# Optimization experiments

Hardware: AMD Instinct MI355X
Metric: run time of the kernel (lower is better)

The kernel has to match this reference:

```python
import jax, jax.numpy as jnp
import numpy as np

N = 100000      # nodes
E = 800000      # edges (avg degree 8)
D_IN = 64
H1 = H2 = H3 = 64
HEADS = 2
D_EDGE = 5
NEG_SLOPE = 0.2  # GATConv leaky_relu slope


def _lin(key, fi, fo):
    kw, kb = jax.random.split(key)
    w = jax.random.normal(kw, (fi, fo), jnp.float32) / np.sqrt(fi)
    b = jax.random.normal(kb, (fo,), jnp.float32) * 0.01
    return w, b


def setup_inputs() -> dict:
    key = jax.random.key(0)
    ks = jax.random.split(key, 16)
    x = jax.random.normal(ks[0], (N, D_IN), jnp.float32)
    edge_index = jax.random.randint(ks[1], (2, E), 0, N, dtype=jnp.int32)
    edge_attr = jax.random.normal(ks[2], (E, D_EDGE), jnp.float32)

    inp = {"x": x, "edge_index": edge_index, "edge_attr": edge_attr}
    dims = [(D_IN, H1), (H1, H2), (H2, H3)]
    for i, (fi, fo) in enumerate(dims, start=1):
        k = jax.random.fold_in(ks[3], i)
        ka, kb, kc = jax.random.split(k, 3)
        inp[f"w_node{i}"], inp[f"b_node{i}"] = _lin(ka, fi, fo)
        inp[f"w_edge{i}"], inp[f"b_edge{i}"] = _lin(kb, D_EDGE, fo)
        inp[f"w_comb{i}"], inp[f"b_comb{i}"] = _lin(kc, 2 * fo, fo)
    # GATConv: shared lin for src/dst, att vectors, bias (concat=False -> size H3)
    kg, ks_, kd, kbias = jax.random.split(ks[4], 4)
    inp["w_gat"] = jax.random.normal(kg, (H3, HEADS * H3), jnp.float32) / np.sqrt(H3)
    inp["att_src"] = jax.random.normal(ks_, (HEADS, H3), jnp.float32) * 0.1
    inp["att_dst"] = jax.random.normal(kd, (HEADS, H3), jnp.float32) * 0.1
    inp["b_gat"] = jax.random.normal(kbias, (H3,), jnp.float32) * 0.01
    return inp


def _edge_conv(h, src, dst, ea, wn, bn, we, be, wc, bc, n):
    # lin_node / lin_edge applied densely, then gather -> concat -> lin -> scatter-add
    hn = h @ wn + bn                       # [N, C]
    ef = ea @ we + be                      # [E, C]
    msg = jnp.concatenate([hn[src], ef], axis=1) @ wc + bc  # [E, C]
    return jax.ops.segment_sum(msg, dst, num_segments=n)


def _gat(h, src, dst, w_gat, att_src, att_dst, b_gat, n):
    g = (h @ w_gat).reshape(n, HEADS, -1)          # [N, H, C]
    a_src = jnp.einsum("nhc,hc->nh", g, att_src)    # [N, H]
    a_dst = jnp.einsum("nhc,hc->nh", g, att_dst)
    alpha = jax.nn.leaky_relu(a_src[src] + a_dst[dst], NEG_SLOPE)  # [E, H]
    # segment softmax over incoming edges of each dst node
    m = jax.ops.segment_max(alpha, dst, num_segments=n)
    alpha = jnp.exp(alpha - m[dst])
    denom = jax.ops.segment_sum(alpha, dst, num_segments=n)
    alpha = alpha / (denom[dst] + 1e-16)
    out = jax.ops.segment_sum(g[src] * alpha[:, :, None], dst, num_segments=n)  # [N,H,C]
    return out.mean(axis=1) + b_gat  # concat=False -> mean over heads, plus bias


def reference(x, edge_index, edge_attr,
              w_node1, b_node1, w_edge1, b_edge1, w_comb1, b_comb1,
              w_node2, b_node2, w_edge2, b_edge2, w_comb2, b_comb2,
              w_node3, b_node3, w_edge3, b_edge3, w_comb3, b_comb3,
              w_gat, att_src, att_dst, b_gat):
    n = x.shape[0]
    src, dst = edge_index[0], edge_index[1]
    h = x
    h = jax.nn.relu(_edge_conv(h, src, dst, edge_attr, w_node1, b_node1, w_edge1, b_edge1, w_comb1, b_comb1, n))
    h = jax.nn.relu(_edge_conv(h, src, dst, edge_attr, w_node2, b_node2, w_edge2, b_edge2, w_comb2, b_comb2, n))
    h = jax.nn.relu(_edge_conv(h, src, dst, edge_attr, w_node3, b_node3, w_edge3, b_edge3, w_comb3, b_comb3, n))
    h = _gat(h, src, dst, w_gat, att_src, att_dst, b_gat, n)
    return h.reshape(-1)  # torch.flatten
```

## Files before the change

kernel.cpp:

```cpp
#include <hip/hip_runtime.h>
#include <hip/hip_fp16.h>
#include <math.h>


#define TPB 256

typedef unsigned int u32;

__device__ inline float2 f16unpack2(u32 u) {
    __half2 h = *reinterpret_cast<__half2*>(&u);
    return __half22float2(h);
}
__device__ inline float4 f16unpack4(uint2 q) {
    float2 a = f16unpack2(q.x), b = f16unpack2(q.y);
    return make_float4(a.x, a.y, b.x, b.y);
}
__device__ inline u32 f16pack2(float lo, float hi) {
    __half2 h = __floats2half2_rn(lo, hi);
    return *reinterpret_cast<u32*>(&h);
}
__device__ inline void fma_f16x8(float* acc, uint4 v, float w) {
    float2 t;
    t = f16unpack2(v.x); acc[0] = fmaf(w, t.x, acc[0]); acc[1] = fmaf(w, t.y, acc[1]);
    t = f16unpack2(v.y); acc[2] = fmaf(w, t.x, acc[2]); acc[3] = fmaf(w, t.y, acc[3]);
    t = f16unpack2(v.z); acc[4] = fmaf(w, t.x, acc[4]); acc[5] = fmaf(w, t.y, acc[5]);
    t = f16unpack2(v.w); acc[6] = fmaf(w, t.x, acc[6]); acc[7] = fmaf(w, t.y, acc[7]);
}
__device__ inline void acc_h16(float4& acc, uint2 v) {
    float2 a = f16unpack2(v.x);
    float2 b = f16unpack2(v.y);
    acc.x += a.x; acc.y += a.y; acc.z += b.x; acc.w += b.y;
}

#define MAC4(acc, a, w0, w1, w2, w3)                                           \
    acc.x = fmaf(a.x, w0.x, acc.x); acc.y = fmaf(a.x, w0.y, acc.y);            \
    acc.z = fmaf(a.x, w0.z, acc.z); acc.w = fmaf(a.x, w0.w, acc.w);            \
    acc.x = fmaf(a.y, w1.x, acc.x); acc.y = fmaf(a.y, w1.y, acc.y);            \
    acc.z = fmaf(a.y, w1.z, acc.z); acc.w = fmaf(a.y, w1.w, acc.w);            \
    acc.x = fmaf(a.z, w2.x, acc.x); acc.y = fmaf(a.z, w2.y, acc.y);            \
    acc.z = fmaf(a.z, w2.z, acc.z); acc.w = fmaf(a.z, w2.w, acc.w);            \
    acc.x = fmaf(a.w, w3.x, acc.x); acc.y = fmaf(a.w, w3.y, acc.y);            \
    acc.z = fmaf(a.w, w3.z, acc.z); acc.w = fmaf(a.w, w3.w, acc.w);

struct CombPtrs {
    const float* wn; const float* bn;
    const float* we; const float* be;
    const float* wc; const float* bc;
    float* W1;
};

__global__ __launch_bounds__(TPB) void k_prep(CombPtrs p0, CombPtrs p1, CombPtrs p2,
                                              const float* __restrict__ wg, u32* __restrict__ wgh,
                                              const float4* __restrict__ X, uint4* __restrict__ XH,
                                              int n8, int nbC,
                                              int* __restrict__ rs, int nz) {
    const int b = blockIdx.x;
    if (b >= 4 + nbC) {
        int i = (b - 4 - nbC) * TPB + threadIdx.x;
        if (i < nz) rs[i] = 0;
        return;
    }
    if (b >= 4) {
        int i = (b - 4) * TPB + threadIdx.x;
        if (i < n8) {
            float4 a = X[i * 2], c = X[i * 2 + 1];
            uint4 o;
            o.x = f16pack2(a.x, a.y); o.y = f16pack2(a.z, a.w);
            o.z = f16pack2(c.x, c.y); o.w = f16pack2(c.z, c.w);
            XH[i] = o;
        }
        return;
    }
    if (b == 3) {
        for (int i = threadIdx.x; i < 4096; i += TPB) {
            float2 v = *(const float2*)&wg[i * 2];
            wgh[i] = f16pack2(v.x, v.y);
        }
        return;
    }
    CombPtrs P = (b == 0) ? p0 : ((b == 1) ? p1 : p2);
    const float* wn = P.wn; const float* bn = P.bn;
    const float* we = P.we; const float* be = P.be;
    const float* wc = P.wc; const float* bc = P.bc;
    float* W1 = P.W1;
    float* W2 = P.W1 + 4096;
    float* cv = P.W1 + 4416;
    int tid = threadIdx.x;
    for (int idx = tid; idx < 64 * 64; idx += TPB) {
        int i = idx >> 6, j = idx & 63;
        float acc = 0.f;
        #pragma unroll 8
        for (int k = 0; k < 64; k++) acc = fmaf(wn[i * 64 + k], wc[k * 64 + j], acc);
        W1[idx] = acc;
    }
    for (int idx = tid; idx < 5 * 64; idx += TPB) {
        int i = idx >> 6, j = idx & 63;
        float acc = 0.f;
        #pragma unroll 8
        for (int k = 0; k < 64; k++) acc = fmaf(we[i * 64 + k], wc[(64 + k) * 64 + j], acc);
        W2[idx] = acc;
    }
    for (int j = tid; j < 64; j += TPB) {
        float acc = bc[j];
        for (int k = 0; k < 64; k++) {
            acc = fmaf(bn[k], wc[k * 64 + j], acc);
            acc = fmaf(be[k], wc[(64 + k) * 64 + j], acc);
        }
        cv[j] = acc;
    }
}

__global__ __launch_bounds__(TPB) void k_hist(const int* __restrict__ dst, int* __restrict__ cnt,
                                              int* __restrict__ rank, int E) {
    int e = blockIdx.x * TPB + threadIdx.x;
    if (e < E) rank[e] = atomicAdd(&cnt[dst[e]], 1);
}

__global__ __launch_bounds__(TPB) void k_scan1(int* __restrict__ data, int* __restrict__ partials, int n) {
    __shared__ int s[TPB];
    int i = blockIdx.x * TPB + threadIdx.x;
    int v = (i < n) ? data[i] : 0;
    s[threadIdx.x] = v;
    __syncthreads();
    for (int off = 1; off < TPB; off <<= 1) {
        int t = (threadIdx.x >= off) ? s[threadIdx.x - off] : 0;
        __syncthreads();
        s[threadIdx.x] += t;
        __syncthreads();
    }
    if (i < n) data[i] = s[threadIdx.x] - v;
    if (threadIdx.x == TPB - 1) partials[blockIdx.x] = s[TPB - 1];
}

__global__ __launch_bounds__(TPB) void k_scan3(int* __restrict__ data, const int* __restrict__ partials,
                                               int n, int total) {
    const int bid = blockIdx.x;
    int s = 0;
    for (int j = threadIdx.x; j < bid; j += TPB) s += partials[j];
    #pragma unroll
    for (int off = 32; off > 0; off >>= 1) s += __shfl_down(s, off);
    __shared__ int ws[4];
    if ((threadIdx.x & 63) == 0) ws[threadIdx.x >> 6] = s;
    __syncthreads();
    int pre = ws[0] + ws[1] + ws[2] + ws[3];
    int i = bid * TPB + threadIdx.x;
    if (i < n) data[i] += pre;
    if (i == 0) data[n] = total;
}

__global__ __launch_bounds__(TPB) void k_scatter(const int* __restrict__ src, const int* __restrict__ dst,
                                                 const int* __restrict__ rank, const int* __restrict__ row_start,
                                                 int2* __restrict__ csr_se, int E) {
    int e = blockIdx.x * TPB + threadIdx.x;
    if (e < E) {
        int idx = row_start[dst[e]] + rank[e];
        csr_se[idx] = make_int2(src[e], e);
    }
}

template <bool IN16, bool OUT16, bool GAT, bool B5C>
__global__ __launch_bounds__(TPB, 6) void k_ec_fused(const void* __restrict__ Hv,
                                                     const int* __restrict__ row_start,
                                                     const int2* __restrict__ csr_se,
                                                     const float* __restrict__ Wfold,
                                                     float* __restrict__ B5,
                                                     const float* __restrict__ EA,
                                                     void* __restrict__ OUTv, int n,
                                                     const u32* __restrict__ Wgh,
                                                     const float* __restrict__ att_src,
                                                     const float* __restrict__ att_dst,
                                                     u32* __restrict__ Gh,
                                                     float* __restrict__ asrc,
                                                     float* __restrict__ adst) {
    __shared__ float Alds[64 * 68];
    __shared__ u32 Wglds[GAT ? 4096 : 4];
    __shared__ float Blds[B5C ? 320 : 4];
    const float* Hf = (const float*)Hv;
    const u32*   Hh = (const u32*)Hv;
    const int t = threadIdx.x;
    const int base = blockIdx.x * 64;

    if (GAT) {
        #pragma unroll
        for (int rep = 0; rep < 4; rep++) {
            int i = rep * 256 + t;
            *(uint4*)&Wglds[i * 4] = ((const uint4*)Wgh)[i];
        }
    }

    const int lane = t & 63;
    const int lid = lane & 15;
    const int gbase = lane & 48;
    const int gid = t >> 4;
    const int c4 = lid * 4;
    const int h2i = lid * 2;
    for (int i = 0; i < 4; i++) {
        int r = gid * 4 + i;
        int node = base + r;
        float4 acc = make_float4(0.f, 0.f, 0.f, 0.f);
        float b0 = 0.f, b1 = 0.f, b2 = 0.f, b3 = 0.f, b4 = 0.f;
        if (node < n) {
            int beg = row_start[node], end = row_start[node + 1];
            for (int chunk = beg; chunk < end; chunk += 16) {
                int cdeg = min(end - chunk, 16);
                bool ev = (chunk + lid < end);
                int2 se = ev ? csr_se[chunk + lid] : make_int2(0, 0);
                int s_l = se.x;
                if (B5C && ev) {
                    const float* p = EA + (size_t)se.y * 5;
                    b0 += p[0]; b1 += p[1]; b2 += p[2]; b3 += p[3]; b4 += p[4];
                }
                int it = 0;
                for (; it + 7 < cdeg; it += 8) {
                    int se0 = __shfl(s_l, gbase + it);
                    int se1 = __shfl(s_l, gbase + it + 1);
                    int se2 = __shfl(s_l, gbase + it + 2);
                    int se3 = __shfl(s_l, gbase + it + 3);
                    int se4 = __shfl(s_l, gbase + it + 4);
                    int se5 = __shfl(s_l, gbase + it + 5);
                    int se6 = __shfl(s_l, gbase + it + 6);
                    int se7 = __shfl(s_l, gbase + it + 7);
                    if (IN16) {
                        uint2 v0 = *(const uint2*)&Hh[(size_t)se0 * 32 + h2i];
                        uint2 v1 = *(const uint2*)&Hh[(size_t)se1 * 32 + h2i];
                        uint2 v2 = *(const uint2*)&Hh[(size_t)se2 * 32 + h2i];
                        uint2 v3 = *(const uint2*)&Hh[(size_t)se3 * 32 + h2i];
                        uint2 v4 = *(const uint2*)&Hh[(size_t)se4 * 32 + h2i];
                        uint2 v5 = *(const uint2*)&Hh[(size_t)se5 * 32 + h2i];
                        uint2 v6 = *(const uint2*)&Hh[(size_t)se6 * 32 + h2i];
                        uint2 v7 = *(const uint2*)&Hh[(size_t)se7 * 32 + h2i];
                        acc_h16(acc, v0); acc_h16(acc, v1); acc_h16(acc, v2); acc_h16(acc, v3);
                        acc_h16(acc, v4); acc_h16(acc, v5); acc_h16(acc, v6); acc_h16(acc, v7);
                    } else {
                        float4 v0 = *(const float4*)&Hf[(size_t)se0 * 64 + c4];
                        float4 v1 = *(const float4*)&Hf[(size_t)se1 * 64 + c4];
                        float4 v2 = *(const float4*)&Hf[(size_t)se2 * 64 + c4];
                        float4 v3 = *(const float4*)&Hf[(size_t)se3 * 64 + c4];
                        float4 v4 = *(const float4*)&Hf[(size_t)se4 * 64 + c4];
                        float4 v5 = *(const float4*)&Hf[(size_t)se5 * 64 + c4];
                        float4 v6 = *(const float4*)&Hf[(size_t)se6 * 64 + c4];
                        float4 v7 = *(const float4*)&Hf[(size_t)se7 * 64 + c4];
                        acc.x += ((v0.x + v1.x) + (v2.x + v3.x)) + ((v4.x + v5.x) + (v6.x + v7.x));
                        acc.y += ((v0.y + v1.y) + (v2.y + v3.y)) + ((v4.y + v5.y) + (v6.y + v7.y));
                        acc.z += ((v0.z + v1.z) + (v2.z + v3.z)) + ((v4.z + v5.z) + (v6.z + v7.z));
                        acc.w += ((v0.w + v1.w) + (v2.w + v3.w)) + ((v4.w + v5.w) + (v6.w + v7.w));
                    }
                }
                for (; it + 3 < cdeg; it += 4) {
                    int se0 = __shfl(s_l, gbase + it);
                    int se1 = __shfl(s_l, gbase + it + 1);
                    int se2 = __shfl(s_l, gbase + it + 2);
                    int se3 = __shfl(s_l, gbase + it + 3);
                    if (IN16) {
                        uint2 v0 = *(const uint2*)&Hh[(size_t)se0 * 32 + h2i];
                        uint2 v1 = *(const uint2*)&Hh[(size_t)se1 * 32 + h2i];
                        uint2 v2 = *(const uint2*)&Hh[(size_t)se2 * 32 + h2i];
                        uint2 v3 = *(const uint2*)&Hh[(size_t)se3 * 32 + h2i];
                        acc_h16(acc, v0); acc_h16(acc, v1); acc_h16(acc, v2); acc_h16(acc, v3);
                    } else {
                        float4 v0 = *(const float4*)&Hf[(size_t)se0 * 64 + c4];
                        float4 v1 = *(const float4*)&Hf[(size_t)se1 * 64 + c4];
                        float4 v2 = *(const float4*)&Hf[(size_t)se2 * 64 + c4];
                        float4 v3 = *(const float4*)&Hf[(size_t)se3 * 64 + c4];
                        acc.x += (v0.x + v1.x) + (v2.x + v3.x);
                        acc.y += (v0.y + v1.y) + (v2.y + v3.y);
                        acc.z += (v0.z + v1.z) + (v2.z + v3.z);
                        acc.w += (v0.w + v1.w) + (v2.w + v3.w);
                    }
                }
                for (; it < cdeg; it++) {
                    int se_ = __shfl(s_l, gbase + it);
                    if (IN16) {
                        uint2 v = *(const uint2*)&Hh[(size_t)se_ * 32 + h2i];
                        acc_h16(acc, v);
                    } else {
                        float4 v = *(const float4*)&Hf[(size_t)se_ * 64 + c4];
                        acc.x += v.x; acc.y += v.y; acc.z += v.z; acc.w += v.w;
                    }
                }
            }
        }
        *(float4*)&Alds[r * 68 + c4] = acc;
        if (B5C) {
            #pragma unroll
            for (int off = 1; off < 16; off <<= 1) {
                b0 += __shfl_xor(b0, off); b1 += __shfl_xor(b1, off);
                b2 += __shfl_xor(b2, off); b3 += __shfl_xor(b3, off);
                b4 += __shfl_xor(b4, off);
            }
            if (lid == 0 && node < n) {
                Blds[r * 5 + 0] = b0; Blds[r * 5 + 1] = b1; Blds[r * 5 + 2] = b2;
                Blds[r * 5 + 3] = b3; Blds[r * 5 + 4] = b4;
                float* bp = B5 + (size_t)node * 5;
                bp[0] = b0; bp[1] = b1; bp[2] = b2; bp[3] = b3; bp[4] = b4;
            }
        }
    }
    __syncthreads();

    const int r0 = (t >> 4) * 4, c0 = (t & 15) * 4;
    float4 acc0 = make_float4(0.f, 0.f, 0.f, 0.f), acc1 = acc0, acc2 = acc0, acc3 = acc0;
    #pragma unroll 2
    for (int k = 0; k < 64; k += 4) {
        float4 a0 = *(float4*)&Alds[(r0 + 0) * 68 + k];
        float4 a1 = *(float4*)&Alds[(r0 + 1) * 68 + k];
        float4 a2 = *(float4*)&Alds[(r0 + 2) * 68 + k];
        float4 a3 = *(float4*)&Alds[(r0 + 3) * 68 + k];
        float4 w0 = *(const float4*)&Wfold[(k + 0) * 64 + c0];
        float4 w1 = *(const float4*)&Wfold[(k + 1) * 64 + c0];
        float4 w2 = *(const float4*)&Wfold[(k + 2) * 64 + c0];
        float4 w3 = *(const float4*)&Wfold[(k + 3) * 64 + c0];
        MAC4(acc0, a0, w0, w1, w2, w3);
        MAC4(acc1, a1, w0, w1, w2, w3);
        MAC4(acc2, a2, w0, w1, w2, w3);
        MAC4(acc3, a3, w0, w1, w2, w3);
    }
    float4 w2c[5];
    #pragma unroll
    for (int j = 0; j < 5; j++) w2c[j] = *(const float4*)&Wfold[4096 + j * 64 + c0];
    const float4 cv4 = *(const float4*)&Wfold[4416 + c0];

    if (GAT) __syncthreads();

    #define EC_STORE(i, acc)                                                        \
        { int row = base + r0 + i;                                                  \
          if (row < n) {                                                            \
              float deg = (float)(row_start[row + 1] - row_start[row]);             \
              float4 q;                                                             \
              q.x = deg * cv4.x; q.y = deg * cv4.y;                                 \
              q.z = deg * cv4.z; q.w = deg * cv4.w;                                 \
              for (int j = 0; j < 5; j++) {                                         \
                  float b = B5C ? Blds[(r0 + i) * 5 + j] : B5[(size_t)row * 5 + j]; \
                  q.x = fmaf(b, w2c[j].x, q.x); q.y = fmaf(b, w2c[j].y, q.y);       \
                  q.z = fmaf(b, w2c[j].z, q.z); q.w = fmaf(b, w2c[j].w, q.w);       \
              }                                                                     \
              float4 r4;                                                            \
              r4.x = fmaxf(acc.x + q.x, 0.f); r4.y = fmaxf(acc.y + q.y, 0.f);       \
              r4.z = fmaxf(acc.z + q.z, 0.f); r4.w = fmaxf(acc.w + q.w, 0.f);       \
              if (GAT) {                                                            \
                  *(float4*)&Alds[(r0 + i) * 68 + c0] = r4;                         \
              } else if (OUT16) {                                                   \
                  u32* O = (u32*)OUTv;                                              \
                  uint2 gg;                                                         \
                  gg.x = f16pack2(r4.x, r4.y); gg.y = f16pack2(r4.z, r4.w);         \
                  *(uint2*)&O[(size_t)row * 32 + (c0 >> 1)] = gg;                   \
              } else {                                                              \
                  float* O = (float*)OUTv;                                          \
                  *(float4*)&O[(size_t)row * 64 + c0] = r4;                         \
              } } }
    EC_STORE(0, acc0) EC_STORE(1, acc1) EC_STORE(2, acc2) EC_STORE(3, acc3)
    #undef EC_STORE

    if (GAT) {
        __syncthreads();
        float4 p00 = make_float4(0.f, 0.f, 0.f, 0.f), p01 = p00, p02 = p00, p03 = p00;
        float4 p10 = p00, p11 = p00, p12 = p00, p13 = p00;
        #pragma unroll 2
        for (int k = 0; k < 64; k += 4) {
            float4 a0 = *(float4*)&Alds[(r0 + 0) * 68 + k];
            float4 a1 = *(float4*)&Alds[(r0 + 1) * 68 + k];
            float4 a2 = *(float4*)&Alds[(r0 + 2) * 68 + k];
            float4 a3 = *(float4*)&Alds[(r0 + 3) * 68 + k];
            float4 u0 = f16unpack4(*(uint2*)&Wglds[(k + 0) * 64 + (c0 >> 1)]);
            float4 u1 = f16unpack4(*(uint2*)&Wglds[(k + 1) * 64 + (c0 >> 1)]);
            float4 u2 = f16unpack4(*(uint2*)&Wglds[(k + 2) * 64 + (c0 >> 1)]);
            float4 u3 = f16unpack4(*(uint2*)&Wglds[(k + 3) * 64 + (c0 >> 1)]);
            MAC4(p00, a0, u0, u1, u2, u3);
            MAC4(p01, a1, u0, u1, u2, u3);
            MAC4(p02, a2, u0, u1, u2, u3);
            MAC4(p03, a3, u0, u1, u2, u3);
            float4 v0 = f16unpack4(*(uint2*)&Wglds[(k + 0) * 64 + 32 + (c0 >> 1)]);
            float4 v1 = f16unpack4(*(uint2*)&Wglds[(k + 1) * 64 + 32 + (c0 >> 1)]);
            float4 v2 = f16unpack4(*(uint2*)&Wglds[(k + 2) * 64 + 32 + (c0 >> 1)]);
            float4 v3 = f16unpack4(*(uint2*)&Wglds[(k + 3) * 64 + 32 + (c0 >> 1)]);
            MAC4(p10, a0, v0, v1, v2, v3);
            MAC4(p11, a1, v0, v1, v2, v3);
            MAC4(p12, a2, v0, v1, v2, v3);
            MAC4(p13, a3, v0, v1, v2, v3);
        }
        const float4 as0 = *(const float4*)&att_src[c0];
        const float4 as1 = *(const float4*)&att_src[64 + c0];
        const float4 ad0 = *(const float4*)&att_dst[c0];
        const float4 ad1 = *(const float4*)&att_dst[64 + c0];
        #define DOT4(a, b) (a.x * b.x + a.y * b.y + a.z * b.z + a.w * b.w)
        #define GAT_ROW(i, h0, h1)                                                      \
            { int row = base + r0 + i;                                                  \
              float s0 = DOT4(h0, as0), s1 = DOT4(h1, as1);                             \
              float d0 = DOT4(h0, ad0), d1 = DOT4(h1, ad1);                             \
              s0 += __shfl_xor(s0, 1); s1 += __shfl_xor(s1, 1);                         \
              d0 += __shfl_xor(d0, 1); d1 += __shfl_xor(d1, 1);                         \
              s0 += __shfl_xor(s0, 2); s1 += __shfl_xor(s1, 2);                         \
              d0 += __shfl_xor(d0, 2); d1 += __shfl_xor(d1, 2);                         \
              s0 += __shfl_xor(s0, 4); s1 += __shfl_xor(s1, 4);                         \
              d0 += __shfl_xor(d0, 4); d1 += __shfl_xor(d1, 4);                         \
              s0 += __shfl_xor(s0, 8); s1 += __shfl_xor(s1, 8);                         \
              d0 += __shfl_xor(d0, 8); d1 += __shfl_xor(d1, 8);                         \
              if (row < n) {                                                            \
                  uint2 g0; g0.x = f16pack2(h0.x, h0.y); g0.y = f16pack2(h0.z, h0.w);   \
                  uint2 g1; g1.x = f16pack2(h1.x, h1.y); g1.y = f16pack2(h1.z, h1.w);   \
                  *(uint2*)&Gh[(size_t)row * 64 + (c0 >> 1)] = g0;                      \
                  *(uint2*)&Gh[(size_t)row * 64 + 32 + (c0 >> 1)] = g1;                 \
                  if ((t & 15) == 0) {                                                  \
                      float2 sv; sv.x = s0; sv.y = s1;                                  \
                      float2 dv; dv.x = d0; dv.y = d1;                                  \
                      *(float2*)&asrc[(size_t)row * 2] = sv;                            \
                      *(float2*)&adst[(size_t)row * 2] = dv; } } }
        GAT_ROW(0, p00, p10) GAT_ROW(1, p01, p11) GAT_ROW(2, p02, p12) GAT_ROW(3, p03, p13)
        #undef GAT_ROW
        #undef DOT4
    }
}

__global__ __launch_bounds__(TPB) void k_gat_agg(const u32* __restrict__ Gh, const int* __restrict__ row_start,
                                                 const int2* __restrict__ csr_se, const float* __restrict__ asrc,
                                                 const float* __restrict__ adst, const float* __restrict__ bgat,
                                                 float* __restrict__ OUT, int n) {
    const int node = blockIdx.x * 16 + (threadIdx.x >> 4);
    if (node >= n) return;
    const int lane = threadIdx.x & 63;
    const int lid = lane & 15;
    const int gbase = lane & 48;
    const int head = lid >> 3;
    const int u4 = lid * 4;
    const int beg = row_start[node], end = row_start[node + 1];
    const float2 adv = *(const float2*)&adst[(size_t)node * 2];
    float m0 = -INFINITY, m1 = -INFINITY, d0 = 0.f, d1 = 0.f;
    float A[8] = {0.f, 0.f, 0.f, 0.f, 0.f, 0.f, 0.f, 0.f};
    for (int chunk = beg; chunk < end; chunk += 16) {
        int cdeg = min(end - chunk, 16);
        bool valid = (lid < cdeg);
        int s_l = valid ? csr_se[chunk + lid].x : 0;
        float al0 = -INFINITY, al1 = -INFINITY;
        if (valid) {
            float2 av = *(const float2*)&asrc[(size_t)s_l * 2];
            float t0 = av.x + adv.x, t1 = av.y + adv.y;
            al0 = (t0 > 0.f) ? t0 : 0.2f * t0;
            al1 = (t1 > 0.f) ? t1 : 0.2f * t1;
        }
        float cm0 = al0, cm1 = al1;
        #pragma unroll
        for (int off = 1; off < 16; off <<= 1) {
            cm0 = fmaxf(cm0, __shfl_xor(cm0, off));
            cm1 = fmaxf(cm1, __shfl_xor(cm1, off));
        }
        float nm0 = fmaxf(m0, cm0), nm1 = fmaxf(m1, cm1);
        float sc0 = __expf(m0 - nm0), sc1 = __expf(m1 - nm1);
        float w0 = valid ? __expf(al0 - nm0) : 0.f;
        float w1 = valid ? __expf(al1 - nm1) : 0.f;
        float cd0 = w0, cd1 = w1;
        #pragma unroll
        for (int off = 1; off < 16; off <<= 1) {
            cd0 += __shfl_xor(cd0, off);
            cd1 += __shfl_xor(cd1, off);
        }
        d0 = d0 * sc0 + cd0;
        d1 = d1 * sc1 + cd1;
        float scsel = head ? sc1 : sc0;
        #pragma unroll
        for (int j = 0; j < 8; j++) A[j] *= scsel;
        m0 = nm0; m1 = nm1;
        int it = 0;
        for (; it + 3 < cdeg; it += 4) {
            int sa = __shfl(s_l, gbase + it);
            int sb = __shfl(s_l, gbase + it + 1);
            int sc = __shfl(s_l, gbase + it + 2);
            int sd = __shfl(s_l, gbase + it + 3);
            float w0a = __shfl(w0, gbase + it),     w1a = __shfl(w1, gbase + it);
            float w0b = __shfl(w0, gbase + it + 1), w1b = __shfl(w1, gbase + it + 1);
            float w0c = __shfl(w0, gbase + it + 2), w1c = __shfl(w1, gbase + it + 2);
            float w0d = __shfl(w0, gbase + it + 3), w1d = __shfl(w1, gbase + it + 3);
            float wa = head ? w1a : w0a;
            float wb = head ? w1b : w0b;
            float wc = head ? w1c : w0c;
            float wd = head ? w1d : w0d;
            uint4 va = *(const uint4*)&Gh[(size_t)sa * 64 + u4];
            uint4 vb = *(const uint4*)&Gh[(size_t)sb * 64 + u4];
            uint4 vc = *(const uint4*)&Gh[(size_t)sc * 64 + u4];
            uint4 vd = *(const uint4*)&Gh[(size_t)sd * 64 + u4];
            fma_f16x8(A, va, wa);
            fma_f16x8(A, vb, wb);
            fma_f16x8(A, vc, wc);
            fma_f16x8(A, vd, wd);
        }
        for (; it + 1 < cdeg; it += 2) {
            int sa = __shfl(s_l, gbase + it);
            int sb = __shfl(s_l, gbase + it + 1);
            float w0a = __shfl(w0, gbase + it),     w1a = __shfl(w1, gbase + it);
            float w0b = __shfl(w0, gbase + it + 1), w1b = __shfl(w1, gbase + it + 1);
            float wa = head ? w1a : w0a;
            float wb = head ? w1b : w0b;
            uint4 va = *(const uint4*)&Gh[(size_t)sa * 64 + u4];
            uint4 vb = *(const uint4*)&Gh[(size_t)sb * 64 + u4];
            fma_f16x8(A, va, wa);
            fma_f16x8(A, vb, wb);
        }
        if (it < cdeg) {
            int sa = __shfl(s_l, gbase + it);
            float w0a = __shfl(w0, gbase + it), w1a = __shfl(w1, gbase + it);
            float wa = head ? w1a : w0a;
            uint4 va = *(const uint4*)&Gh[(size_t)sa * 64 + u4];
            fma_f16x8(A, va, wa);
        }
    }
    float rh = 0.5f / ((head ? d1 : d0) + 1e-16f);
    #pragma unroll
    for (int j = 0; j < 8; j++) {
        A[j] *= rh;
        A[j] += __shfl_xor(A[j], 8);
    }
    if (head == 0) {
        int cb = (lid & 7) * 8;
        const float4 bg0 = *(const float4*)&bgat[cb];
        const float4 bg1 = *(const float4*)&bgat[cb + 4];
        float4 o0; o0.x = A[0] + bg0.x; o0.y = A[1] + bg0.y; o0.z = A[2] + bg0.z; o0.w = A[3] + bg0.w;
        float4 o1; o1.x = A[4] + bg1.x; o1.y = A[5] + bg1.y; o1.z = A[6] + bg1.z; o1.w = A[7] + bg1.w;
        float* op = &OUT[(size_t)node * 64 + cb];
        *(float4*)op = o0;
        *(float4*)(op + 4) = o1;
    }
}

extern "C" void kernel_launch(void* const* d_in, const int* in_sizes, int n_in,
                              void* d_out, int out_size, void* d_ws, size_t ws_size,
                              hipStream_t stream) {
    const float* x   = (const float*)d_in[0];
    const int*   ei  = (const int*)d_in[1];
    const float* ea  = (const float*)d_in[2];
    const int N = in_sizes[0] / 64;
    const int E = in_sizes[1] / 2;
    const int* src = ei;
    const int* dst = ei + E;

    const float* wn[3] = {(const float*)d_in[3],  (const float*)d_in[9],  (const float*)d_in[15]};
    const float* bn[3] = {(const float*)d_in[4],  (const float*)d_in[10], (const float*)d_in[16]};
    const float* we[3] = {(const float*)d_in[5],  (const float*)d_in[11], (const float*)d_in[17]};
    const float* be[3] = {(const float*)d_in[6],  (const float*)d_in[12], (const float*)d_in[18]};
    const float* wc[3] = {(const float*)d_in[7],  (const float*)d_in[13], (const float*)d_in[19]};
    const float* bc[3] = {(const float*)d_in[8],  (const float*)d_in[14], (const float*)d_in[20]};
    const float* wgat    = (const float*)d_in[21];
    const float* att_src = (const float*)d_in[22];
    const float* att_dst = (const float*)d_in[23];
    const float* bgat    = (const float*)d_in[24];

    char* ws = (char*)d_ws;
    size_t off = 0;
    auto alloc = [&](size_t bytes) -> void* {
        void* p = ws + off;
        off = (off + bytes + 255) & ~(size_t)255;
        return p;
    };
    int*   row_start = (int*)alloc((size_t)(N + 1) * 4);
    int*   partials  = (int*)alloc(1024 * 4);
    int*   rank      = (int*)alloc((size_t)E * 4);
    int2*  csr_se    = (int2*)alloc((size_t)E * 8);
    float* Wc        = (float*)alloc((size_t)3 * 4480 * 4);
    u32*   Wgh       = (u32*)alloc((size_t)4096 * 4);
    float* B5        = (float*)alloc((size_t)N * 5 * 4);
    u32*   xh        = (u32*)alloc((size_t)N * 64 * 2);
    u32*   bufH0     = (u32*)alloc((size_t)N * 64 * 2);
    u32*   bufH1     = (u32*)alloc((size_t)N * 64 * 2);
    u32*   Gh        = (u32*)alloc((size_t)N * 64 * 4);
    float* asrc      = (float*)alloc((size_t)N * 2 * 4);
    float* adst      = (float*)alloc((size_t)N * 2 * 4);
    float* out = (float*)d_out;

    const int nbN = (N + TPB - 1) / TPB;
    const int nbE = (E + TPB - 1) / TPB;
    const int grpBlocks = (N + 15) / 16;
    const int tiles = (N + 63) / 64;
    const int n8 = N * 8;
    const int nbC = (n8 + TPB - 1) / TPB;
    const int nbZ = (N + 1 + TPB - 1) / TPB;

    CombPtrs p0 = {wn[0], bn[0], we[0], be[0], wc[0], bc[0], Wc};
    CombPtrs p1 = {wn[1], bn[1], we[1], be[1], wc[1], bc[1], Wc + 4480};
    CombPtrs p2 = {wn[2], bn[2], we[2], be[2], wc[2], bc[2], Wc + 2 * 4480};
    k_prep<<<4 + nbC + nbZ, TPB, 0, stream>>>(p0, p1, p2, wgat, Wgh,
                                              (const float4*)x, (uint4*)xh, n8, nbC,
                                              row_start, N + 1);

    k_hist<<<nbE, TPB, 0, stream>>>(dst, row_start, rank, E);
    k_scan1<<<nbN, TPB, 0, stream>>>(row_start, partials, N);
    k_scan3<<<nbN, TPB, 0, stream>>>(row_start, partials, N, E);
    k_scatter<<<nbE, TPB, 0, stream>>>(src, dst, rank, row_start, csr_se, E);

    k_ec_fused<true, true, false, true><<<tiles, TPB, 0, stream>>>(
        xh,    row_start, csr_se, Wc,            B5, ea, bufH0, N,
        nullptr, nullptr, nullptr, nullptr, nullptr, nullptr);
    k_ec_fused<true, true, false, false><<<tiles, TPB, 0, stream>>>(
        bufH0, row_start, csr_se, Wc + 4480,     B5, nullptr, bufH1, N,
        nullptr, nullptr, nullptr, nullptr, nullptr, nullptr);
    k_ec_fused<true, true, true, false><<<tiles, TPB, 0, stream>>>(
        bufH1, row_start, csr_se, Wc + 2 * 4480, B5, nullptr, nullptr, N,
        Wgh, att_src, att_dst, Gh, asrc, adst);

    k_gat_agg<<<grpBlocks, TPB, 0, stream>>>(Gh, row_start, csr_se, asrc, adst, bgat, out, N);
}
```

Baseline: 408.7 us.

## Aggregate 64-wide features before GAT projection and fold attention vectors into weights

Result: slower. 457.9 us (+12.0%).

```diff
diff --git a/kernel.cpp b/kernel.cpp
--- a/kernel.cpp
+++ b/kernel.cpp
@@ -18,13 +18,6 @@
 __device__ inline u32 f16pack2(float lo, float hi) {
     __half2 h = __floats2half2_rn(lo, hi);
     return *reinterpret_cast<u32*>(&h);
-}
-__device__ inline void fma_f16x8(float* acc, uint4 v, float w) {
-    float2 t;
-    t = f16unpack2(v.x); acc[0] = fmaf(w, t.x, acc[0]); acc[1] = fmaf(w, t.y, acc[1]);
-    t = f16unpack2(v.y); acc[2] = fmaf(w, t.x, acc[2]); acc[3] = fmaf(w, t.y, acc[3]);
-    t = f16unpack2(v.z); acc[4] = fmaf(w, t.x, acc[4]); acc[5] = fmaf(w, t.y, acc[5]);
-    t = f16unpack2(v.w); acc[6] = fmaf(w, t.x, acc[6]); acc[7] = fmaf(w, t.y, acc[7]);
 }
 __device__ inline void acc_h16(float4& acc, uint2 v) {
     float2 a = f16unpack2(v.x);
@@ -51,6 +44,9 @@
 
 __global__ __launch_bounds__(TPB) void k_prep(CombPtrs p0, CombPtrs p1, CombPtrs p2,
                                               const float* __restrict__ wg, u32* __restrict__ wgh,
+                                              const float* __restrict__ att_src,
+                                              const float* __restrict__ att_dst,
+                                              float* __restrict__ vsd,
                                               const float4* __restrict__ X, uint4* __restrict__ XH,
                                               int n8, int nbC,
                                               int* __restrict__ rs, int nz) {
@@ -75,6 +71,17 @@
         for (int i = threadIdx.x; i < 4096; i += TPB) {
             float2 v = *(const float2*)&wg[i * 2];
             wgh[i] = f16pack2(v.x, v.y);
+        }
+        {
+            int i = threadIdx.x;
+            int type = i >> 6, k = i & 63;
+            int h = type & 1, sd = type >> 1;
+            const float* att = (sd ? att_dst : att_src) + h * 64;
+            const float* wrow = wg + k * 128 + h * 64;
+            float acc = 0.f;
+            #pragma unroll 8
+            for (int c = 0; c < 64; c++) acc = fmaf(wrow[c], att[c], acc);
+            vsd[type * 64 + k] = acc;
         }
         return;
     }
@@ -158,7 +165,7 @@
     }
 }
 
-template <bool IN16, bool OUT16, bool GAT, bool B5C>
+template <bool IN16, bool OUT16, bool SCORES, bool B5C>
 __global__ __launch_bounds__(TPB, 6) void k_ec_fused(const void* __restrict__ Hv,
                                                      const int* __restrict__ row_start,
                                                      const int2* __restrict__ csr_se,
@@ -166,27 +173,15 @@
                                                      float* __restrict__ B5,
                                                      const float* __restrict__ EA,
                                                      void* __restrict__ OUTv, int n,
-                                                     const u32* __restrict__ Wgh,
-                                                     const float* __restrict__ att_src,
-                                                     const float* __restrict__ att_dst,
-                                                     u32* __restrict__ Gh,
+                                                     const float* __restrict__ vsd,
                                                      float* __restrict__ asrc,
                                                      float* __restrict__ adst) {
     __shared__ float Alds[64 * 68];
-    __shared__ u32 Wglds[GAT ? 4096 : 4];
     __shared__ float Blds[B5C ? 320 : 4];
     const float* Hf = (const float*)Hv;
     const u32*   Hh = (const u32*)Hv;
     const int t = threadIdx.x;
     const int base = blockIdx.x * 64;
-
-    if (GAT) {
-        #pragma unroll
-        for (int rep = 0; rep < 4; rep++) {
-            int i = rep * 256 + t;
-            *(uint4*)&Wglds[i * 4] = ((const uint4*)Wgh)[i];
-        }
-    }
 
     const int lane = t & 63;
     const int lid = lane & 15;
@@ -319,9 +314,15 @@
     #pragma unroll
     for (int j = 0; j < 5; j++) w2c[j] = *(const float4*)&Wfold[4096 + j * 64 + c0];
     const float4 cv4 = *(const float4*)&Wfold[4416 + c0];
-
-    if (GAT) __syncthreads();
-
+    float4 vs0, vs1, vd0, vd1;
+    if (SCORES) {
+        vs0 = *(const float4*)&vsd[0 * 64 + c0];
+        vs1 = *(const float4*)&vsd[1 * 64 + c0];
+        vd0 = *(const float4*)&vsd[2 * 64 + c0];
+        vd1 = *(const float4*)&vsd[3 * 64 + c0];
+    }
+
+    #define DOT4(a, b) (a.x * b.x + a.y * b.y + a.z * b.z + a.w * b.w)
     #define EC_STORE(i, acc)                                                        \
         { int row = base + r0 + i;                                                  \
           if (row < n) {                                                            \
@@ -337,9 +338,25 @@
               float4 r4;                                                            \
               r4.x = fmaxf(acc.x + q.x, 0.f); r4.y = fmaxf(acc.y + q.y, 0.f);       \
               r4.z = fmaxf(acc.z + q.z, 0.f); r4.w = fmaxf(acc.w + q.w, 0.f);       \
-              if (GAT) {                                                            \
-                  *(float4*)&Alds[(r0 + i) * 68 + c0] = r4;                         \
-              } else if (OUT16) {                                                   \
+              if (SCORES) {                                                         \
+                  float s0 = DOT4(r4, vs0), s1 = DOT4(r4, vs1);                     \
+                  float d0 = DOT4(r4, vd0), d1 = DOT4(r4, vd1);                     \
+                  s0 += __shfl_xor(s0, 1); s1 += __shfl_xor(s1, 1);                 \
+                  d0 += __shfl_xor(d0, 1); d1 += __shfl_xor(d1, 1);                 \
+                  s0 += __shfl_xor(s0, 2); s1 += __shfl_xor(s1, 2);                 \
+                  d0 += __shfl_xor(d0, 2); d1 += __shfl_xor(d1, 2);                 \
+                  s0 += __shfl_xor(s0, 4); s1 += __shfl_xor(s1, 4);                 \
+                  d0 += __shfl_xor(d0, 4); d1 += __shfl_xor(d1, 4);                 \
+                  s0 += __shfl_xor(s0, 8); s1 += __shfl_xor(s1, 8);                 \
+                  d0 += __shfl_xor(d0, 8); d1 += __shfl_xor(d1, 8);                 \
+                  if ((t & 15) == 0) {                                              \
+                      float2 sv; sv.x = s0; sv.y = s1;                              \
+                      float2 dv; dv.x = d0; dv.y = d1;                              \
+                      *(float2*)&asrc[(size_t)row * 2] = sv;                        \
+                      *(float2*)&adst[(size_t)row * 2] = dv;                        \
+                  }                                                                 \
+              }                                                                     \
+              if (OUT16) {                                                          \
                   u32* O = (u32*)OUTv;                                              \
                   uint2 gg;                                                         \
                   gg.x = f16pack2(r4.x, r4.y); gg.y = f16pack2(r4.z, r4.w);         \
@@ -350,82 +367,36 @@
               } } }
     EC_STORE(0, acc0) EC_STORE(1, acc1) EC_STORE(2, acc2) EC_STORE(3, acc3)
     #undef EC_STORE
-
-    if (GAT) {
-        __syncthreads();
-        float4 p00 = make_float4(0.f, 0.f, 0.f, 0.f), p01 = p00, p02 = p00, p03 = p00;
-        float4 p10 = p00, p11 = p00, p12 = p00, p13 = p00;
-        #pragma unroll 2
-        for (int k = 0; k < 64; k += 4) {
-            float4 a0 = *(float4*)&Alds[(r0 + 0) * 68 + k];
-            float4 a1 = *(float4*)&Alds[(r0 + 1) * 68 + k];
-            float4 a2 = *(float4*)&Alds[(r0 + 2) * 68 + k];
-            float4 a3 = *(float4*)&Alds[(r0 + 3) * 68 + k];
-            float4 u0 = f16unpack4(*(uint2*)&Wglds[(k + 0) * 64 + (c0 >> 1)]);
-            float4 u1 = f16unpack4(*(uint2*)&Wglds[(k + 1) * 64 + (c0 >> 1)]);
-            float4 u2 = f16unpack4(*(uint2*)&Wglds[(k + 2) * 64 + (c0 >> 1)]);
-            float4 u3 = f16unpack4(*(uint2*)&Wglds[(k + 3) * 64 + (c0 >> 1)]);
-            MAC4(p00, a0, u0, u1, u2, u3);
-            MAC4(p01, a1, u0, u1, u2, u3);
-            MAC4(p02, a2, u0, u1, u2, u3);
-            MAC4(p03, a3, u0, u1, u2, u3);
-            float4 v0 = f16unpack4(*(uint2*)&Wglds[(k + 0) * 64 + 32 + (c0 >> 1)]);
-            float4 v1 = f16unpack4(*(uint2*)&Wglds[(k + 1) * 64 + 32 + (c0 >> 1)]);
-            float4 v2 = f16unpack4(*(uint2*)&Wglds[(k + 2) * 64 + 32 + (c0 >> 1)]);
-            float4 v3 = f16unpack4(*(uint2*)&Wglds[(k + 3) * 64 + 32 + (c0 >> 1)]);
-            MAC4(p10, a0, v0, v1, v2, v3);
-            MAC4(p11, a1, v0, v1, v2, v3);
-            MAC4(p12, a2, v0, v1, v2, v3);
-            MAC4(p13, a3, v0, v1, v2, v3);
-        }
-        const float4 as0 = *(const float4*)&att_src[c0];
-        const float4 as1 = *(const float4*)&att_src[64 + c0];
-        const float4 ad0 = *(const float4*)&att_dst[c0];
-        const float4 ad1 = *(const float4*)&att_dst[64 + c0];
-        #define DOT4(a, b) (a.x * b.x + a.y * b.y + a.z * b.z + a.w * b.w)
-        #define GAT_ROW(i, h0, h1)                                                      \
-            { int row = base + r0 + i;                                                  \
-              float s0 = DOT4(h0, as0), s1 = DOT4(h1, as1);                             \
-              float d0 = DOT4(h0, ad0), d1 = DOT4(h1, ad1);                             \
-              s0 += __shfl_xor(s0, 1); s1 += __shfl_xor(s1, 1);                         \
-              d0 += __shfl_xor(d0, 1); d1 += __shfl_xor(d1, 1);                         \
-              s0 += __shfl_xor(s0, 2); s1 += __shfl_xor(s1, 2);                         \
-              d0 += __shfl_xor(d0, 2); d1 += __shfl_xor(d1, 2);                         \
-              s0 += __shfl_xor(s0, 4); s1 += __shfl_xor(s1, 4);                         \
-              d0 += __shfl_xor(d0, 4); d1 += __shfl_xor(d1, 4);                         \
-              s0 += __shfl_xor(s0, 8); s1 += __shfl_xor(s1, 8);                         \
-              d0 += __shfl_xor(d0, 8); d1 += __shfl_xor(d1, 8);                         \
-              if (row < n) {                                                            \
-                  uint2 g0; g0.x = f16pack2(h0.x, h0.y); g0.y = f16pack2(h0.z, h0.w);   \
-                  uint2 g1; g1.x = f16pack2(h1.x, h1.y); g1.y = f16pack2(h1.z, h1.w);   \
-                  *(uint2*)&Gh[(size_t)row * 64 + (c0 >> 1)] = g0;                      \
-                  *(uint2*)&Gh[(size_t)row * 64 + 32 + (c0 >> 1)] = g1;                 \
-                  if ((t & 15) == 0) {                                                  \
-                      float2 sv; sv.x = s0; sv.y = s1;                                  \
-                      float2 dv; dv.x = d0; dv.y = d1;                                  \
-                      *(float2*)&asrc[(size_t)row * 2] = sv;                            \
-                      *(float2*)&adst[(size_t)row * 2] = dv; } } }
-        GAT_ROW(0, p00, p10) GAT_ROW(1, p01, p11) GAT_ROW(2, p02, p12) GAT_ROW(3, p03, p13)
-        #undef GAT_ROW
-        #undef DOT4
-    }
-}
-
-__global__ __launch_bounds__(TPB) void k_gat_agg(const u32* __restrict__ Gh, const int* __restrict__ row_start,
-                                                 const int2* __restrict__ csr_se, const float* __restrict__ asrc,
-                                                 const float* __restrict__ adst, const float* __restrict__ bgat,
+    #undef DOT4
+}
+
+__global__ __launch_bounds__(TPB) void k_gat_agg(const u32* __restrict__ Hh,
+                                                 const int* __restrict__ row_start,
+                                                 const int2* __restrict__ csr_se,
+                                                 const float* __restrict__ asrc,
+                                                 const float* __restrict__ adst,
+                                                 const u32* __restrict__ Wgh,
+                                                 const float* __restrict__ bgat,
                                                  float* __restrict__ OUT, int n) {
-    const int node = blockIdx.x * 16 + (threadIdx.x >> 4);
-    if (node >= n) return;
-    const int lane = threadIdx.x & 63;
+    __shared__ float Ash[16][2][68];
+    const int t = threadIdx.x;
+    const int g = t >> 4;
+    const int node = blockIdx.x * 16 + g;
+    const int lane = t & 63;
     const int lid = lane & 15;
     const int gbase = lane & 48;
-    const int head = lid >> 3;
-    const int u4 = lid * 4;
-    const int beg = row_start[node], end = row_start[node + 1];
-    const float2 adv = *(const float2*)&adst[(size_t)node * 2];
+    const int h2i = lid * 2;
+    const bool active = (node < n);
+
     float m0 = -INFINITY, m1 = -INFINITY, d0 = 0.f, d1 = 0.f;
-    float A[8] = {0.f, 0.f, 0.f, 0.f, 0.f, 0.f, 0.f, 0.f};
+    float A0[4] = {0.f, 0.f, 0.f, 0.f};
+    float A1[4] = {0.f, 0.f, 0.f, 0.f};
+    int beg = 0, end = 0;
+    float2 adv = make_float2(0.f, 0.f);
+    if (active) {
+        beg = row_start[node]; end = row_start[node + 1];
+        adv = *(const float2*)&adst[(size_t)node * 2];
+    }
     for (int chunk = beg; chunk < end; chunk += 16) {
         int cdeg = min(end - chunk, 16);
         bool valid = (lid < cdeg);
@@ -455,9 +426,8 @@
         }
         d0 = d0 * sc0 + cd0;
         d1 = d1 * sc1 + cd1;
-        float scsel = head ? sc1 : sc0;
         #pragma unroll
-        for (int j = 0; j < 8; j++) A[j] *= scsel;
+        for (int j = 0; j < 4; j++) { A0[j] *= sc0; A1[j] *= sc1; }
         m0 = nm0; m1 = nm1;
         int it = 0;
         for (; it + 3 < cdeg; it += 4) {
@@ -469,54 +439,62 @@
             float w0b = __shfl(w0, gbase + it + 1), w1b = __shfl(w1, gbase + it + 1);
             float w0c = __shfl(w0, gbase + it + 2), w1c = __shfl(w1, gbase + it + 2);
             float w0d = __shfl(w0, gbase + it + 3), w1d = __shfl(w1, gbase + it + 3);
-            float wa = head ? w1a : w0a;
-            float wb = head ? w1b : w0b;
-            float wc = head ? w1c : w0c;
-            float wd = head ? w1d : w0d;
-            uint4 va = *(const uint4*)&Gh[(size_t)sa * 64 + u4];
-            uint4 vb = *(const uint4*)&Gh[(size_t)sb * 64 + u4];
-            uint4 vc = *(const uint4*)&Gh[(size_t)sc * 64 + u4];
-            uint4 vd = *(const uint4*)&Gh[(size_t)sd * 64 + u4];
-            fma_f16x8(A, va, wa);
-            fma_f16x8(A, vb, wb);
-            fma_f16x8(A, vc, wc);
-            fma_f16x8(A, vd, wd);
-        }
-        for (; it + 1 < cdeg; it += 2) {
-            int sa = __shfl(s_l, gbase + it);
-            int sb = __shfl(s_l, gbase + it + 1);
-            float w0a = __shfl(w0, gbase + it),     w1a = __shfl(w1, gbase + it);
-            float w0b = __shfl(w0, gbase + it + 1), w1b = __shfl(w1, gbase + it + 1);
-            float wa = head ? w1a : w0a;
-            float wb = head ? w1b : w0b;
-            uint4 va = *(const uint4*)&Gh[(size_t)sa * 64 + u4];
-            uint4 vb = *(const uint4*)&Gh[(size_t)sb * 64 + u4];
-            fma_f16x8(A, va, wa);
-            fma_f16x8(A, vb, wb);
-        }
-        if (it < cdeg) {
+            float4 ha = f16unpack4(*(const uint2*)&Hh[(size_t)sa * 32 + h2i]);
+            float4 hb = f16unpack4(*(const uint2*)&Hh[(size_t)sb * 32 + h2i]);
+            float4 hc = f16unpack4(*(const uint2*)&Hh[(size_t)sc * 32 + h2i]);
+            float4 hd = f16unpack4(*(const uint2*)&Hh[(size_t)sd * 32 + h2i]);
+            A0[0] = fmaf(w0a, ha.x, A0[0]); A1[0] = fmaf(w1a, ha.x, A1[0]);
+            A0[1] = fmaf(w0a, ha.y, A0[1]); A1[1] = fmaf(w1a, ha.y, A1[1]);
+            A0[2] = fmaf(w0a, ha.z, A0[2]); A1[2] = fmaf(w1a, ha.z, A1[2]);
+            A0[3] = fmaf(w0a, ha.w, A0[3]); A1[3] = fmaf(w1a, ha.w, A1[3]);
+            A0[0] = fmaf(w0b, hb.x, A0[0]); A1[0] = fmaf(w1b, hb.x, A1[0]);
+            A0[1] = fmaf(w0b, hb.y, A0[1]); A1[1] = fmaf(w1b, hb.y, A1[1]);
+            A0[2] = fmaf(w0b, hb.z, A0[2]); A1[2] = fmaf(w1b, hb.z, A1[2]);
+            A0[3] = fmaf(w0b, hb.w, A0[3]); A1[3] = fmaf(w1b, hb.w, A1[3]);
+            A0[0] = fmaf(w0c, hc.x, A0[0]); A1[0] = fmaf(w1c, hc.x, A1[0]);
+            A0[1] = fmaf(w0c, hc.y, A0[1]); A1[1] = fmaf(w1c, hc.y, A1[1]);
+            A0[2] = fmaf(w0c, hc.z, A0[2]); A1[2] = fmaf(w1c, hc.z, A1[2]);
+            A0[3] = fmaf(w0c, hc.w, A0[3]); A1[3] = fmaf(w1c, hc.w, A1[3]);
+            A0[0] = fmaf(w0d, hd.x, A0[0]); A1[0] = fmaf(w1d, hd.x, A1[0]);
+            A0[1] = fmaf(w0d, hd.y, A0[1]); A1[1] = fmaf(w1d, hd.y, A1[1]);
+            A0[2] = fmaf(w0d, hd.z, A0[2]); A1[2] = fmaf(w1d, hd.z, A1[2]);
+            A0[3] = fmaf(w0d, hd.w, A0[3]); A1[3] = fmaf(w1d, hd.w, A1[3]);
+        }
+        for (; it < cdeg; it++) {
             int sa = __shfl(s_l, gbase + it);
             float w0a = __shfl(w0, gbase + it), w1a = __shfl(w1, gbase + it);
-            float wa = head ? w1a : w0a;
-            uint4 va = *(const uint4*)&Gh[(size_t)sa * 64 + u4];
-            fma_f16x8(A, va, wa);
-        }
-    }
-    float rh = 0.5f / ((head ? d1 : d0) + 1e-16f);
+            float4 ha = f16unpack4(*(const uint2*)&Hh[(size_t)sa * 32 + h2i]);
+            A0[0] = fmaf(w0a, ha.x, A0[0]); A1[0] = fmaf(w1a, ha.x, A1[0]);
+            A0[1] = fmaf(w0a, ha.y, A0[1]); A1[1] = fmaf(w1a, ha.y, A1[1]);
+            A0[2] = fmaf(w0a, ha.z, A0[2]); A1[2] = fmaf(w1a, ha.z, A1[2]);
+            A0[3] = fmaf(w0a, ha.w, A0[3]); A1[3] = fmaf(w1a, ha.w, A1[3]);
+        }
+    }
+    float r0s = 0.5f / (d0 + 1e-16f);
+    float r1s = 0.5f / (d1 + 1e-16f);
     #pragma unroll
-    for (int j = 0; j < 8; j++) {
-        A[j] *= rh;
-        A[j] += __shfl_xor(A[j], 8);
-    }
-    if (head == 0) {
-        int cb = (lid & 7) * 8;
-        const float4 bg0 = *(const float4*)&bgat[cb];
-        const float4 bg1 = *(const float4*)&bgat[cb + 4];
-        float4 o0; o0.x = A[0] + bg0.x; o0.y = A[1] + bg0.y; o0.z = A[2] + bg0.z; o0.w = A[3] + bg0.w;
-        float4 o1; o1.x = A[4] + bg1.x; o1.y = A[5] + bg1.y; o1.z = A[6] + bg1.z; o1.w = A[7] + bg1.w;
-        float* op = &OUT[(size_t)node * 64 + cb];
-        *(float4*)op = o0;
-        *(float4*)(op + 4) = o1;
+    for (int j = 0; j < 4; j++) {
+        Ash[g][0][lid * 4 + j] = A0[j] * r0s;
+        Ash[g][1][lid * 4 + j] = A1[j] * r1s;
+    }
+    __syncthreads();
+
+    if (active) {
+        const int c0 = (t & 15) * 4;
+        const float4 bg = *(const float4*)&bgat[c0];
+        float4 acc = bg;
+        #pragma unroll 4
+        for (int k = 0; k < 64; k++) {
+            float a0 = Ash[g][0][k];
+            float a1 = Ash[g][1][k];
+            float4 w0v = f16unpack4(*(const uint2*)&Wgh[k * 64 + (c0 >> 1)]);
+            float4 w1v = f16unpack4(*(const uint2*)&Wgh[k * 64 + 32 + (c0 >> 1)]);
+            acc.x = fmaf(a0, w0v.x, acc.x); acc.y = fmaf(a0, w0v.y, acc.y);
+            acc.z = fmaf(a0, w0v.z, acc.z); acc.w = fmaf(a0, w0v.w, acc.w);
+            acc.x = fmaf(a1, w1v.x, acc.x); acc.y = fmaf(a1, w1v.y, acc.y);
+            acc.z = fmaf(a1, w1v.z, acc.z); acc.w = fmaf(a1, w1v.w, acc.w);
+        }
+        *(float4*)&OUT[(size_t)node * 64 + c0] = acc;
     }
 }
 
@@ -555,11 +533,11 @@
     int2*  csr_se    = (int2*)alloc((size_t)E * 8);
     float* Wc        = (float*)alloc((size_t)3 * 4480 * 4);
     u32*   Wgh       = (u32*)alloc((size_t)4096 * 4);
+    float* vsd       = (float*)alloc((size_t)256 * 4);
     float* B5        = (float*)alloc((size_t)N * 5 * 4);
     u32*   xh        = (u32*)alloc((size_t)N * 64 * 2);
     u32*   bufH0     = (u32*)alloc((size_t)N * 64 * 2);
     u32*   bufH1     = (u32*)alloc((size_t)N * 64 * 2);
-    u32*   Gh        = (u32*)alloc((size_t)N * 64 * 4);
     float* asrc      = (float*)alloc((size_t)N * 2 * 4);
     float* adst      = (float*)alloc((size_t)N * 2 * 4);
     float* out = (float*)d_out;
@@ -576,6 +554,7 @@
     CombPtrs p1 = {wn[1], bn[1], we[1], be[1], wc[1], bc[1], Wc + 4480};
     CombPtrs p2 = {wn[2], bn[2], we[2], be[2], wc[2], bc[2], Wc + 2 * 4480};
     k_prep<<<4 + nbC + nbZ, TPB, 0, stream>>>(p0, p1, p2, wgat, Wgh,
+                                              att_src, att_dst, vsd,
                                               (const float4*)x, (uint4*)xh, n8, nbC,
                                               row_start, N + 1);
 
@@ -586,13 +565,14 @@
 
     k_ec_fused<true, true, false, true><<<tiles, TPB, 0, stream>>>(
         xh,    row_start, csr_se, Wc,            B5, ea, bufH0, N,
-        nullptr, nullptr, nullptr, nullptr, nullptr, nullptr);
+        nullptr, nullptr, nullptr);
     k_ec_fused<true, true, false, false><<<tiles, TPB, 0, stream>>>(
         bufH0, row_start, csr_se, Wc + 4480,     B5, nullptr, bufH1, N,
-        nullptr, nullptr, nullptr, nullptr, nullptr, nullptr);
+        nullptr, nullptr, nullptr);
     k_ec_fused<true, true, true, false><<<tiles, TPB, 0, stream>>>(
-        bufH1, row_start, csr_se, Wc + 2 * 4480, B5, nullptr, nullptr, N,
-        Wgh, att_src, att_dst, Gh, asrc, adst);
-
-    k_gat_agg<<<grpBlocks, TPB, 0, stream>>>(Gh, row_start, csr_se, asrc, adst, bgat, out, N);
-}
+        bufH1, row_start, csr_se, Wc + 2 * 4480, B5, nullptr, bufH0, N,
+        vsd, asrc, adst);
+
+    k_gat_agg<<<grpBlocks, TPB, 0, stream>>>(bufH0, row_start, csr_se, asrc, adst,
+                                             Wgh, bgat, out, N);
+}
```
